# Kernel optimization log

Measured on AMD Instinct MI355X. Metric: run time of the kernel, lower is better.

Reference implementation:

```python
import jax, jax.numpy as jnp
import numpy as np
import math

B, S, D = 2, 2048, 1024
E = 1024          # dim_embedds
H = 16            # num_heads
DK = E // H       # d_k = 64


def _xavier(key, shape):
    fan_out, fan_in = shape
    limit = math.sqrt(6.0 / (fan_in + fan_out))
    return jax.random.uniform(key, shape, jnp.float32, -limit, limit)


def setup_inputs() -> dict:
    key = jax.random.key(0)
    k_x, k_qkv, k_o = jax.random.split(key, 3)
    return {
        "x": jax.random.normal(k_x, (B, S, D), jnp.float32),
        "W_qkv": _xavier(k_qkv, (3 * E, D)),   # torch Linear weight [out, in]
        "b_qkv": jnp.zeros((3 * E,), jnp.float32),
        "W_o": _xavier(k_o, (E, E)),
        "b_o": jnp.zeros((E,), jnp.float32),
    }


def reference(x, W_qkv, b_qkv, W_o, b_o):
    b, s, _ = x.shape
    # fused QKV projection: [B,S,3E] -> [B,S,H,3,DK] (per-head interleaved q,k,v)
    qkv = (jnp.einsum("bsd,ed->bse", x, W_qkv) + b_qkv).reshape(b, s, H, 3, DK)
    qkv = jnp.transpose(qkv, (3, 0, 2, 1, 4))  # [3,B,H,S,DK]
    q, k, v = qkv[0], qkv[1], qkv[2]
    scores = jnp.einsum("bhqd,bhkd->bhqk", q, k) / math.sqrt(DK)  # [B,H,S,S]
    attn = jax.nn.softmax(scores, axis=-1)
    out = jnp.einsum("bhqk,bhkd->bhqd", attn, v)  # [B,H,S,DK]
    out = jnp.transpose(out, (0, 2, 1, 3)).reshape(b, s, E)  # combine heads
    return jnp.einsum("bse,fe->bsf", out, W_o) + b_o
```

## Files before the change

### kernel.cpp

```cpp
#include <hip/hip_runtime.h>
#include <stdint.h>


typedef unsigned short u16;
typedef unsigned int u32;
typedef __attribute__((ext_vector_type(8))) short bf16x8;
typedef __attribute__((ext_vector_type(4))) float f32x4;
typedef __attribute__((ext_vector_type(4))) unsigned int u32x4;
typedef __attribute__((ext_vector_type(4))) unsigned short u16x4;
typedef __attribute__((ext_vector_type(2))) unsigned int u32x2;

#define LOG2E 1.44269504088896340736f
#define NSHIFT -17.312340490667562f

static __device__ __forceinline__ float bf2f(u16 u) {
  union { u32 u; float f; } v; v.u = ((u32)u) << 16; return v.f;
}
static __device__ __forceinline__ u16 f2bf(float f) {
  union { float f; u32 u; } v; v.f = f;
  return (u16)((v.u + 0x7FFFu + ((v.u >> 16) & 1u)) >> 16);
}
static __device__ __forceinline__ u32 pack2bf(u32 lo, u32 hi) {
  return __builtin_amdgcn_perm(hi, lo, 0x07060302u);
}

static __device__ __forceinline__ void async16(const u16* g, u16* l) {
  __builtin_amdgcn_global_load_lds((const __attribute__((address_space(1))) void*)g,
                                   (__attribute__((address_space(3))) void*)l, 16, 0, 0);
}

static __device__ __forceinline__ bf16x8 ld8cv(const void* p, size_t e, bool isf32) {
  bf16x8 r;
  if (isf32) {
    const u32x4 a = *(const u32x4*)((const float*)p + e);
    const u32x4 b = *(const u32x4*)((const float*)p + e + 4);
    u32* rr = (u32*)&r;
    rr[0] = pack2bf(a[0] + 0x8000u, a[1] + 0x8000u);
    rr[1] = pack2bf(a[2] + 0x8000u, a[3] + 0x8000u);
    rr[2] = pack2bf(b[0] + 0x8000u, b[1] + 0x8000u);
    rr[3] = pack2bf(b[2] + 0x8000u, b[3] + 0x8000u);
  } else {
    r = *(const bf16x8*)((const u16*)p + e);
  }
  return r;
}
static __device__ __forceinline__ float ldscalar(const void* p, int i, bool isf32) {
  return isf32 ? ((const float*)p)[i] : bf2f(((const u16*)p)[i]);
}

__global__ void detect_dtype(const u16* __restrict__ x, u32* __restrict__ flag) {
  const int lane = threadIdx.x & 63;
  const u16 v = x[lane * 2];
  const int e = (v >> 7) & 0xFF;
  const unsigned long long m = __ballot(e >= 100 && e <= 140);
  if (lane == 0) *flag = (__popcll(m) < 48) ? 1u : 0u;
}

__global__ void convert_all(const void* __restrict__ x,  const void* __restrict__ wq,
                            const void* __restrict__ bq, const void* __restrict__ wo,
                            const void* __restrict__ bo,
                            u16* __restrict__ xd, u16* __restrict__ wqd,
                            u16* __restrict__ bqd, u16* __restrict__ wod,
                            u16* __restrict__ bod, const u32* __restrict__ dflag) {
  const bool f32in = (*dflag != 0u);
  const int b = blockIdx.x;
  const void* src; u16* dst; size_t base;
  if (b < 4096)      { src = x;  dst = xd;  base = (size_t)b * 256; }
  else if (b < 7168) { src = wq; dst = wqd; base = (size_t)(b - 4096) * 256; }
  else if (b < 7171) { src = bq; dst = bqd; base = (size_t)(b - 7168) * 256; }
  else if (b < 8195) { src = wo; dst = wod; base = (size_t)(b - 7171) * 256; }
  else               { src = bo; dst = bod; base = 0; }
  const size_t i = base + threadIdx.x;
  if (f32in) {
    const u32x4 a = ((const u32x4*)src)[i];
    u32x2 o;
    o[0] = pack2bf(a[0] + 0x8000u, a[1] + 0x8000u);
    o[1] = pack2bf(a[2] + 0x8000u, a[3] + 0x8000u);
    ((u32x2*)dst)[i] = o;
  } else {
    ((u16x4*)dst)[i] = ((const u16x4*)src)[i];
  }
}

template <int MODE, bool BPRE>
__global__ __launch_bounds__(256, 3) void gemm_nt(
    const u16* __restrict__ A, const void* __restrict__ Bw,
    const void* __restrict__ bias, int K, int N,
    void* __restrict__ out0, u16* __restrict__ out1, u16* __restrict__ out2,
    const u32* __restrict__ dflag)
{
  __shared__ __align__(16) u16 As[128 * 32];
  __shared__ __align__(16) u16 Bs[128 * 32];

  const bool f32in = (*dflag != 0u);
  const bool bw32  = BPRE ? false : f32in;

  const int tid  = threadIdx.x;
  const int wave = tid >> 6, lane = tid & 63;
  const int wm = wave >> 1, wn = wave & 1;
  const int fr = lane & 15, fq = lane >> 4;
  const int m0 = blockIdx.x * 128, n0 = blockIdx.y * 128;

  const u16* gA0 = A + (size_t)(m0 + wave * 32 + (lane >> 2)) * K + (lane & 3) * 8;
  const u16* gA1 = gA0 + (size_t)16 * K;
  u16* lA = As + wave * 1024;

  const u16* gB0 = (const u16*)Bw + (size_t)(n0 + wave * 32 + (lane >> 2)) * K + (lane & 3) * 8;
  const u16* gB1 = gB0 + (size_t)16 * K;
  u16* lB = Bs + wave * 1024;

  const int srow = tid >> 2, scol = (tid & 3) * 8;
  const int li   = srow * 32 + scol;
  const size_t eB = (size_t)(n0 + srow) * K + scol;
  const size_t half = (size_t)64 * K;

  f32x4 acc[4][4];
#pragma unroll
  for (int i = 0; i < 4; ++i)
#pragma unroll
    for (int j = 0; j < 4; ++j) acc[i][j] = (f32x4){0.f, 0.f, 0.f, 0.f};

  for (int kt = 0; kt < K; kt += 32) {
    if (BPRE) {
      __syncthreads();
      async16(gA0, lA);
      async16(gA1, lA + 512);
      async16(gB0, lB);
      async16(gB1, lB + 512);
      gA0 += 32; gA1 += 32; gB0 += 32; gB1 += 32;
      __syncthreads();
    } else {
      const bf16x8 b0 = ld8cv(Bw, eB + kt,        bw32);
      const bf16x8 b1 = ld8cv(Bw, eB + half + kt, bw32);
      __syncthreads();
      async16(gA0, lA);
      async16(gA1, lA + 512);
      gA0 += 32; gA1 += 32;
      *(bf16x8*)(Bs + li)        = b0;
      *(bf16x8*)(Bs + li + 2048) = b1;
      __syncthreads();
    }

    bf16x8 af[4], bfv[4];
#pragma unroll
    for (int mi = 0; mi < 4; ++mi)
      af[mi] = *(const bf16x8*)(As + (wm * 64 + mi * 16 + fr) * 32 + fq * 8);
#pragma unroll
    for (int ni = 0; ni < 4; ++ni)
      bfv[ni] = *(const bf16x8*)(Bs + (wn * 64 + ni * 16 + fr) * 32 + fq * 8);
#pragma unroll
    for (int mi = 0; mi < 4; ++mi)
#pragma unroll
      for (int ni = 0; ni < 4; ++ni)
        acc[mi][ni] = __builtin_amdgcn_mfma_f32_16x16x32_bf16(af[mi], bfv[ni], acc[mi][ni], 0, 0, 0);
  }

  if (MODE == 0) {
    u16* q_out = (u16*)out0;
#pragma unroll
    for (int ni = 0; ni < 4; ++ni) {
      const int eb = n0 + wn * 64 + ni * 16;
      const int h = eb / 192;
      const int rem = eb - h * 192;
      const int which = rem >> 6;
      const int dk = (rem & 63) + fr;
      const float bv = ldscalar(bias, eb + fr, bw32);
#pragma unroll
      for (int mi = 0; mi < 4; ++mi) {
#pragma unroll
        for (int r = 0; r < 4; ++r) {
          const int m = m0 + wm * 64 + mi * 16 + fq * 4 + r;
          const int bb = m >> 11, s = m & 2047;
          const int bh = bb * 16 + h;
          const float v = acc[mi][ni][r] + bv;
          if (which == 0)
            q_out[((size_t)bh * 2048 + s) * 64 + dk] = f2bf(v * 0.125f);
          else if (which == 1)
            out1[((size_t)bh * 2048 + s) * 64 + dk] = f2bf(v);
          else
            out2[((size_t)bh * 64 + dk) * 2048 + s] = f2bf(v);
        }
      }
    }
  } else {
#pragma unroll
    for (int ni = 0; ni < 4; ++ni) {
      const int e = n0 + wn * 64 + ni * 16 + fr;
      const float bv = ldscalar(bias, e, bw32);
#pragma unroll
      for (int mi = 0; mi < 4; ++mi) {
#pragma unroll
        for (int r = 0; r < 4; ++r) {
          const int m = m0 + wm * 64 + mi * 16 + fq * 4 + r;
          const float v = acc[mi][ni][r] + bv;
          if (f32in) ((float*)out0)[(size_t)m * N + e] = v;
          else       ((u16*)out0)[(size_t)m * N + e]   = f2bf(v);
        }
      }
    }
  }
}

__global__ __launch_bounds__(256, 3) void flash_attn(
    const u16* __restrict__ Q, const u16* __restrict__ Kk,
    const u16* __restrict__ Vt, u16* __restrict__ AO)
{
  constexpr int LD = 72;
  __shared__ __align__(16) u16 Kt[64 * LD];
  __shared__ __align__(16) u16 Vl[64 * LD];
  __shared__ __align__(16) u16 Plt[4 * 16 * LD];

  const int tid  = threadIdx.x;
  const int wave = tid >> 6, lane = tid & 63;
  const int fr = lane & 15, fq = lane >> 4;
  const int bh = blockIdx.y;
  const int q0 = blockIdx.x * 64;
  const size_t base = (size_t)bh * 2048 * 64;

  bf16x8 qf[2];
  {
    const u16* qrow = Q + base + (size_t)(q0 + wave * 16 + fr) * 64 + fq * 8;
    qf[0] = *(const bf16x8*)(qrow);
    qf[1] = *(const bf16x8*)(qrow + 32);
  }

  f32x4 oacc[4];
#pragma unroll
  for (int i = 0; i < 4; ++i) oacc[i] = (f32x4){0.f, 0.f, 0.f, 0.f};
  float lacc = 0.f;

  const int srow = tid >> 3, scol = (tid & 7) * 8;
  const int li   = srow * LD + scol;
  const u16* gK = Kk + base + (size_t)srow * 64 + scol;
  const u16* gV = Vt + base + (size_t)srow * 2048 + scol;
  u16* pw = Plt + wave * 16 * LD;

  for (int kt = 0; kt < 32; ++kt) {
    const bf16x8 k0 = *(const bf16x8*)(gK);
    const bf16x8 k1 = *(const bf16x8*)(gK + 32 * 64);
    const bf16x8 v0 = *(const bf16x8*)(gV);
    const bf16x8 v1 = *(const bf16x8*)(gV + 32 * 2048);
    gK += 64 * 64;
    gV += 64;
    __syncthreads();
    *(bf16x8*)(Kt + li)           = k0;
    *(bf16x8*)(Kt + li + 32 * LD) = k1;
    *(bf16x8*)(Vl + li)           = v0;
    *(bf16x8*)(Vl + li + 32 * LD) = v1;
    __syncthreads();

    f32x4 sacc[4];
#pragma unroll
    for (int cb = 0; cb < 4; ++cb) sacc[cb] = (f32x4){0.f, 0.f, 0.f, 0.f};
#pragma unroll
    for (int cb = 0; cb < 4; ++cb) {
      bf16x8 kf0 = *(const bf16x8*)(Kt + (cb * 16 + fr) * LD + fq * 8);
      bf16x8 kf1 = *(const bf16x8*)(Kt + (cb * 16 + fr) * LD + 32 + fq * 8);
      sacc[cb] = __builtin_amdgcn_mfma_f32_16x16x32_bf16(kf0, qf[0], sacc[cb], 0, 0, 0);
      sacc[cb] = __builtin_amdgcn_mfma_f32_16x16x32_bf16(kf1, qf[1], sacc[cb], 0, 0, 0);
    }

#pragma unroll
    for (int cb = 0; cb < 4; ++cb) {
      u32 pb[4];
#pragma unroll
      for (int r = 0; r < 4; ++r) {
        const float pv = exp2f(fmaf(sacc[cb][r], LOG2E, NSHIFT));
        lacc += pv;
        pb[r] = __float_as_uint(pv) + 0x8000u;
      }
      u32x2 pk;
      pk[0] = pack2bf(pb[0], pb[1]);
      pk[1] = pack2bf(pb[2], pb[3]);
      *(u32x2*)(pw + fr * LD + cb * 16 + fq * 4) = pk;
    }

#pragma unroll
    for (int g = 0; g < 2; ++g) {
      bf16x8 pf = *(const bf16x8*)(pw + fr * LD + g * 32 + fq * 8);
#pragma unroll
      for (int db = 0; db < 4; ++db) {
        bf16x8 vf = *(const bf16x8*)(Vl + (db * 16 + fr) * LD + g * 32 + fq * 8);
        oacc[db] = __builtin_amdgcn_mfma_f32_16x16x32_bf16(vf, pf, oacc[db], 0, 0, 0);
      }
    }
  }

  lacc += __shfl_xor(lacc, 16);
  lacc += __shfl_xor(lacc, 32);

  const int b = bh >> 4, h = bh & 15;
  const int s = q0 + wave * 16 + fr;
  const float inv = 1.0f / lacc;
  u16* orow = AO + ((size_t)(b * 2048 + s)) * 1024 + h * 64;
#pragma unroll
  for (int db = 0; db < 4; ++db) {
    u16x4 ov;
#pragma unroll
    for (int r = 0; r < 4; ++r) ov[r] = f2bf(oacc[db][r] * inv);
    *(u16x4*)(orow + db * 16 + fq * 4) = ov;
  }
}

extern "C" void kernel_launch(void* const* d_in, const int* in_sizes, int n_in,
                              void* d_out, int out_size, void* d_ws, size_t ws_size,
                              hipStream_t stream) {
  const void* x    = d_in[0];
  const void* Wqkv = d_in[1];
  const void* bqkv = d_in[2];
  const void* Wo   = d_in[3];
  const void* bo   = d_in[4];

  const size_t HEADS = 32, S = 2048, DK = 64;
  const size_t NQ = HEADS * S * DK;
  u16* Qs = (u16*)d_ws;
  u16* Ks = Qs + NQ;
  u16* Vt = Ks + NQ;
  u16* XA = Vt + NQ;

  u16* Wqb = XA + 2 * S * 1024;
  u16* Wob = Wqb + 3145728;
  u16* bqb = Wob + 1048576;
  u16* bob = bqb + 3072;
  const size_t need_big = ((size_t)(bob + 1024 + 2) - (size_t)d_ws);
  const bool big = ws_size >= need_big;

  u32* flag = big ? (u32*)(bob + 1024) : (u32*)(XA + 2 * S * 1024);

  detect_dtype<<<1, 64, 0, stream>>>((const u16*)x, flag);

  if (big) {
    convert_all<<<8196, 256, 0, stream>>>(x, Wqkv, bqkv, Wo, bo,
                                          XA, Wqb, bqb, Wob, bob, flag);
    gemm_nt<0, true><<<dim3(32, 24), 256, 0, stream>>>(XA, Wqb, bqb, 1024, 3072,
                                                       Qs, Ks, Vt, flag);
    flash_attn<<<dim3(32, 32), 256, 0, stream>>>(Qs, Ks, Vt, XA);
    gemm_nt<1, true><<<dim3(32, 8), 256, 0, stream>>>(XA, Wob, bob, 1024, 1024,
                                                      d_out, nullptr, nullptr, flag);
  } else {
    convert_all<<<4096, 256, 0, stream>>>(x, Wqkv, bqkv, Wo, bo,
                                          XA, XA, XA, XA, XA, flag);
    gemm_nt<0, false><<<dim3(32, 24), 256, 0, stream>>>(XA, Wqkv, bqkv, 1024, 3072,
                                                        Qs, Ks, Vt, flag);
    flash_attn<<<dim3(32, 32), 256, 0, stream>>>(Qs, Ks, Vt, XA);
    gemm_nt<1, false><<<dim3(32, 8), 256, 0, stream>>>(XA, Wo, bo, 1024, 1024,
                                                       d_out, nullptr, nullptr, flag);
  }
}
```

Measured before the change: 219.4 us.

## Stage QKV epilogue through LDS for vectorized stores and drop dtype-detect kernel

The QKV GEMM epilogue now transposes each wave's 16-row accumulator tile through shared memory, so Q/K and the transposed V are written as 16-byte row stores instead of scattered 2-byte writes. The separate detect_dtype launch is removed and each kernel sniffs the input dtype inline with a ballot. The 0.125 Q scale is folded into the weight and bias conversion when the pre-converted weights are used. This cuts a kernel launch and uncoalesced global stores, at the cost of an extra LDS round trip, more syncs and redundant sniffing in every block.

Measured after the change: 208.7 us. -4.9%, faster.

```diff
diff --git a/kernel.cpp b/kernel.cpp
--- a/kernel.cpp
+++ b/kernel.cpp
@@ -22,6 +22,14 @@
 }
 static __device__ __forceinline__ u32 pack2bf(u32 lo, u32 hi) {
   return __builtin_amdgcn_perm(hi, lo, 0x07060302u);
+}
+
+static __device__ __forceinline__ bool sniff_f32(const u16* __restrict__ x) {
+  const int lane = threadIdx.x & 63;
+  const u16 v = x[lane * 2];
+  const int e = (v >> 7) & 0xFF;
+  const unsigned long long m = __ballot(e >= 100 && e <= 140);
+  return __popcll(m) < 48;
 }
 
 static __device__ __forceinline__ void async16(const u16* g, u16* l) {
@@ -48,37 +56,38 @@
   return isf32 ? ((const float*)p)[i] : bf2f(((const u16*)p)[i]);
 }
 
-__global__ void detect_dtype(const u16* __restrict__ x, u32* __restrict__ flag) {
-  const int lane = threadIdx.x & 63;
-  const u16 v = x[lane * 2];
-  const int e = (v >> 7) & 0xFF;
-  const unsigned long long m = __ballot(e >= 100 && e <= 140);
-  if (lane == 0) *flag = (__popcll(m) < 48) ? 1u : 0u;
-}
-
 __global__ void convert_all(const void* __restrict__ x,  const void* __restrict__ wq,
                             const void* __restrict__ bq, const void* __restrict__ wo,
                             const void* __restrict__ bo,
                             u16* __restrict__ xd, u16* __restrict__ wqd,
                             u16* __restrict__ bqd, u16* __restrict__ wod,
-                            u16* __restrict__ bod, const u32* __restrict__ dflag) {
-  const bool f32in = (*dflag != 0u);
+                            u16* __restrict__ bod) {
+  const bool f32in = sniff_f32((const u16*)x);
   const int b = blockIdx.x;
-  const void* src; u16* dst; size_t base;
+  const void* src; u16* dst; size_t base; int seg = 0;
   if (b < 4096)      { src = x;  dst = xd;  base = (size_t)b * 256; }
-  else if (b < 7168) { src = wq; dst = wqd; base = (size_t)(b - 4096) * 256; }
-  else if (b < 7171) { src = bq; dst = bqd; base = (size_t)(b - 7168) * 256; }
+  else if (b < 7168) { src = wq; dst = wqd; base = (size_t)(b - 4096) * 256; seg = 1; }
+  else if (b < 7171) { src = bq; dst = bqd; base = (size_t)(b - 7168) * 256; seg = 2; }
   else if (b < 8195) { src = wo; dst = wod; base = (size_t)(b - 7171) * 256; }
   else               { src = bo; dst = bod; base = 0; }
   const size_t i = base + threadIdx.x;
+  float scale = 1.f;
+  if (seg == 1) { const u32 row = (u32)(i >> 8); if (row % 192u < 64u) scale = 0.125f; }
+  else if (seg == 2) { if (((u32)(i * 4)) % 192u < 64u) scale = 0.125f; }
   if (f32in) {
-    const u32x4 a = ((const u32x4*)src)[i];
-    u32x2 o;
-    o[0] = pack2bf(a[0] + 0x8000u, a[1] + 0x8000u);
-    o[1] = pack2bf(a[2] + 0x8000u, a[3] + 0x8000u);
+    const f32x4 a = ((const f32x4*)src)[i];
+    u32 pb[4];
+#pragma unroll
+    for (int j = 0; j < 4; ++j) pb[j] = __float_as_uint(a[j] * scale) + 0x8000u;
+    u32x2 o; o[0] = pack2bf(pb[0], pb[1]); o[1] = pack2bf(pb[2], pb[3]);
     ((u32x2*)dst)[i] = o;
   } else {
-    ((u16x4*)dst)[i] = ((const u16x4*)src)[i];
+    u16x4 v = ((const u16x4*)src)[i];
+    if (scale != 1.f) {
+#pragma unroll
+      for (int j = 0; j < 4; ++j) v[j] = f2bf(bf2f(v[j]) * scale);
+    }
+    ((u16x4*)dst)[i] = v;
   }
 }
 
@@ -87,12 +96,13 @@
     const u16* __restrict__ A, const void* __restrict__ Bw,
     const void* __restrict__ bias, int K, int N,
     void* __restrict__ out0, u16* __restrict__ out1, u16* __restrict__ out2,
-    const u32* __restrict__ dflag)
+    const u16* __restrict__ xsniff)
 {
-  __shared__ __align__(16) u16 As[128 * 32];
-  __shared__ __align__(16) u16 Bs[128 * 32];
-
-  const bool f32in = (*dflag != 0u);
+  __shared__ __align__(16) u16 smem[8192];
+  u16* As = smem;
+  u16* Bs = smem + 4096;
+
+  const bool f32in = sniff_f32(xsniff);
   const bool bw32  = BPRE ? false : f32in;
 
   const int tid  = threadIdx.x;
@@ -156,29 +166,54 @@
   }
 
   if (MODE == 0) {
-    u16* q_out = (u16*)out0;
-#pragma unroll
-    for (int ni = 0; ni < 4; ++ni) {
-      const int eb = n0 + wn * 64 + ni * 16;
-      const int h = eb / 192;
-      const int rem = eb - h * 192;
-      const int which = rem >> 6;
-      const int dk = (rem & 63) + fr;
-      const float bv = ldscalar(bias, eb + fr, bw32);
+    __syncthreads();
+    u16* swT = smem + wave * 1152;
+    const int region = blockIdx.y * 2 + wn;
+    const int h = region / 3, which = region % 3;
+    float bvv[4];
+#pragma unroll
+    for (int ni = 0; ni < 4; ++ni)
+      bvv[ni] = ldscalar(bias, region * 64 + ni * 16 + fr, bw32);
+    const float qs = BPRE ? 1.f : 0.125f;
+
+    if (which < 2) {
+      u16* outp = (which == 0) ? (u16*)out0 : out1;
+      const float sc = (which == 0) ? qs : 1.f;
 #pragma unroll
       for (int mi = 0; mi < 4; ++mi) {
 #pragma unroll
-        for (int r = 0; r < 4; ++r) {
-          const int m = m0 + wm * 64 + mi * 16 + fq * 4 + r;
+        for (int ni = 0; ni < 4; ++ni)
+#pragma unroll
+          for (int r = 0; r < 4; ++r)
+            swT[(fq * 4 + r) * 72 + ni * 16 + fr] = f2bf((acc[mi][ni][r] + bvv[ni]) * sc);
+#pragma unroll
+        for (int u = 0; u < 2; ++u) {
+          const int idx = u * 64 + lane;
+          const int m_l = idx >> 3, dkc = idx & 7;
+          const bf16x8 row = *(const bf16x8*)(swT + m_l * 72 + dkc * 8);
+          const int m = m0 + wm * 64 + mi * 16 + m_l;
           const int bb = m >> 11, s = m & 2047;
-          const int bh = bb * 16 + h;
-          const float v = acc[mi][ni][r] + bv;
-          if (which == 0)
-            q_out[((size_t)bh * 2048 + s) * 64 + dk] = f2bf(v * 0.125f);
-          else if (which == 1)
-            out1[((size_t)bh * 2048 + s) * 64 + dk] = f2bf(v);
-          else
-            out2[((size_t)bh * 64 + dk) * 2048 + s] = f2bf(v);
+          *(bf16x8*)(outp + ((size_t)(bb * 16 + h) * 2048 + s) * 64 + dkc * 8) = row;
+        }
+      }
+    } else {
+#pragma unroll
+      for (int ni = 0; ni < 4; ++ni) {
+#pragma unroll
+        for (int mi = 0; mi < 4; ++mi) {
+          u16x4 pk;
+#pragma unroll
+          for (int r = 0; r < 4; ++r) pk[r] = f2bf(acc[mi][ni][r] + bvv[ni]);
+          *(u16x4*)(swT + fr * 72 + mi * 16 + fq * 4) = pk;
+        }
+#pragma unroll
+        for (int u = 0; u < 2; ++u) {
+          const int idx = u * 64 + lane;
+          const int dk_l = idx >> 3, mc = idx & 7;
+          const bf16x8 row = *(const bf16x8*)(swT + dk_l * 72 + mc * 8);
+          const int mb = m0 + wm * 64 + mc * 8;
+          const int bb = mb >> 11, s0 = mb & 2047;
+          *(bf16x8*)(out2 + ((size_t)((bb * 16 + h) * 64 + ni * 16 + dk_l)) * 2048 + s0) = row;
         }
       }
     }
@@ -310,6 +345,7 @@
   const void* bqkv = d_in[2];
   const void* Wo   = d_in[3];
   const void* bo   = d_in[4];
+  const u16* xs    = (const u16*)x;
 
   const size_t HEADS = 32, S = 2048, DK = 64;
   const size_t NQ = HEADS * S * DK;
@@ -322,28 +358,24 @@
   u16* Wob = Wqb + 3145728;
   u16* bqb = Wob + 1048576;
   u16* bob = bqb + 3072;
-  const size_t need_big = ((size_t)(bob + 1024 + 2) - (size_t)d_ws);
+  const size_t need_big = ((size_t)(bob + 1024) - (size_t)d_ws);
   const bool big = ws_size >= need_big;
-
-  u32* flag = big ? (u32*)(bob + 1024) : (u32*)(XA + 2 * S * 1024);
-
-  detect_dtype<<<1, 64, 0, stream>>>((const u16*)x, flag);
 
   if (big) {
     convert_all<<<8196, 256, 0, stream>>>(x, Wqkv, bqkv, Wo, bo,
-                                          XA, Wqb, bqb, Wob, bob, flag);
+                                          XA, Wqb, bqb, Wob, bob);
     gemm_nt<0, true><<<dim3(32, 24), 256, 0, stream>>>(XA, Wqb, bqb, 1024, 3072,
-                                                       Qs, Ks, Vt, flag);
+                                                       Qs, Ks, Vt, xs);
     flash_attn<<<dim3(32, 32), 256, 0, stream>>>(Qs, Ks, Vt, XA);
     gemm_nt<1, true><<<dim3(32, 8), 256, 0, stream>>>(XA, Wob, bob, 1024, 1024,
-                                                      d_out, nullptr, nullptr, flag);
+                                                      d_out, nullptr, nullptr, xs);
   } else {
     convert_all<<<4096, 256, 0, stream>>>(x, Wqkv, bqkv, Wo, bo,
-                                          XA, XA, XA, XA, XA, flag);
+                                          XA, XA, XA, XA, XA);
     gemm_nt<0, false><<<dim3(32, 24), 256, 0, stream>>>(XA, Wqkv, bqkv, 1024, 3072,
-                                                        Qs, Ks, Vt, flag);
+                                                        Qs, Ks, Vt, xs);
     flash_attn<<<dim3(32, 32), 256, 0, stream>>>(Qs, Ks, Vt, XA);
     gemm_nt<1, false><<<dim3(32, 8), 256, 0, stream>>>(XA, Wo, bo, 1024, 1024,
-                                                       d_out, nullptr, nullptr, flag);
-  }
-}
+                                                       d_out, nullptr, nullptr, xs);
+  }
+}
```
